# Optimization experiments

Hardware: AMD Instinct MI355X
Metric: run time of the kernel (lower is better)

## Reference

```python
import jax, jax.numpy as jnp
import numpy as np
import math

N_BITS = 8
NUM_GROUPS = 32
NUM_HEADS = 8
EPS = 1e-5


def fake_quant(x):
    # UniformAffineQuantizer: dynamic per-tensor asymmetric 8-bit fake quant
    levels = 2 ** N_BITS - 1
    xmin = jnp.minimum(x.min(), 0.0)
    xmax = jnp.maximum(x.max(), 0.0)
    scale = jnp.maximum((xmax - xmin) / levels, 1e-8)
    zp = jnp.round(-xmin / scale)
    xq = jnp.clip(jnp.round(x / scale) + zp, 0, levels)
    return (xq - zp) * scale


def group_norm(x, w, b):
    # x: (B, C, T)
    B, C, T = x.shape
    xg = x.reshape(B, NUM_GROUPS, C // NUM_GROUPS, T)
    mean = xg.mean(axis=(2, 3), keepdims=True)
    var = xg.var(axis=(2, 3), keepdims=True)
    xg = (xg - mean) * jax.lax.rsqrt(var + EPS)
    return xg.reshape(B, C, T) * w[None, :, None] + b[None, :, None]


def setup_inputs() -> dict:
    key = jax.random.key(0)
    ks = jax.random.split(key, 7)
    C = 512
    x = jax.random.normal(ks[0], (8, C, 32, 32), dtype=jnp.float32)
    gn_w = jnp.ones((C,), jnp.float32)
    gn_b = jnp.zeros((C,), jnp.float32)
    qkv_w = jax.random.normal(ks[1], (3 * C, C), jnp.float32) * (1.0 / math.sqrt(C))
    qkv_b = jax.random.normal(ks[2], (3 * C,), jnp.float32) * 0.01
    proj_w = jax.random.normal(ks[3], (C, C), jnp.float32) * (1.0 / math.sqrt(C))
    proj_b = jax.random.normal(ks[4], (C,), jnp.float32) * 0.01
    return {"x": x, "gn_w": gn_w, "gn_b": gn_b, "qkv_w": qkv_w,
            "qkv_b": qkv_b, "proj_w": proj_w, "proj_b": proj_b}


def reference(x, gn_w, gn_b, qkv_w, qkv_b, proj_w, proj_b):
    b, c, *spatial = x.shape
    T = int(np.prod(spatial))
    xf = x.reshape(b, c, T)                       # (B, C, T)
    h = group_norm(xf, gn_w, gn_b)
    qkv = jnp.einsum('oc,bct->bot', qkv_w, h) + qkv_b[None, :, None]  # (B, 3C, T)
    qkv = qkv.reshape(b * NUM_HEADS, -1, T)       # (B*H, 3*ch, T)
    ch = qkv.shape[1] // 3
    q, k, v = jnp.split(qkv, 3, axis=1)
    q = fake_quant(q)
    k = fake_quant(k)
    v = fake_quant(v)
    scale = 1.0 / math.sqrt(math.sqrt(ch))
    w = jnp.einsum('bct,bcs->bts', q * scale, k * scale)
    w = jax.nn.softmax(w.astype(jnp.float32), axis=-1).astype(q.dtype)
    a = jnp.einsum('bts,bcs->bct', w, v)          # (B*H, ch, T)
    a = a.reshape(b, c, T)
    a = jnp.einsum('oc,bct->bot', proj_w, a) + proj_b[None, :, None]
    return (xf + a).reshape(b, c, *spatial)
```

## Files before the change

### kernel.cpp

```cpp
#include <hip/hip_runtime.h>

typedef __attribute__((ext_vector_type(8))) __bf16 bf16x8;
typedef __attribute__((ext_vector_type(4))) __bf16 bf16x4;
typedef __attribute__((ext_vector_type(4))) float  f32x4;


static constexpr size_t QKV_OFF = 0;
static constexpr size_t HT_OFF  = 50331648;
static constexpr size_t WQ_OFF  = HT_OFF + 8388608;
static constexpr size_t WP_OFF  = WQ_OFF + 1572864;
static constexpr size_t MM_OFF  = WP_OFF + 524288;
static constexpr size_t GST_OFF = MM_OFF + 12288;
static constexpr size_t KI_OFF  = MM_OFF + 16384;
static constexpr size_t VI_OFF  = KI_OFF + 8388608;
static constexpr size_t NEED_NEW = VI_OFF + 8388608;

__device__ __forceinline__ float dqi(float x, float inv_s, float zp) {
    float y = rintf(x * inv_s);
    return fminf(fmaxf(y, -zp), 255.0f - zp);
}
__device__ __forceinline__ f32x4 mfma16(bf16x8 a, bf16x8 b, f32x4 c) {
    return __builtin_amdgcn_mfma_f32_16x16x32_bf16(a, b, c, 0, 0, 0);
}
__device__ __forceinline__ float exp2i(float x) {
    float r;
    asm("v_exp_f32 %0, %1" : "=v"(r) : "v"(x));
    return r;
}
__device__ __forceinline__ void glds16(const __bf16* g, __bf16* l) {
    __builtin_amdgcn_global_load_lds((const __attribute__((address_space(1))) void*)g,
                                     (__attribute__((address_space(3))) void*)l, 16, 0, 0);
}
template <int N> __device__ __forceinline__ void waitv() {
    asm volatile("s_waitcnt vmcnt(%0)" :: "n"(N) : "memory");
}
__device__ __forceinline__ void bar_raw() {
    asm volatile("s_barrier" ::: "memory");
}

__device__ __forceinline__ void red_mm(const float* __restrict__ pmm, int id, int tid,
                                       float* sred, float& mn_out, float& mx_out) {
    const float* p = pmm + id * 1024;
    float mn = fminf(p[tid * 2],     p[(tid + 256) * 2]);
    float mx = fmaxf(p[tid * 2 + 1], p[(tid + 256) * 2 + 1]);
#pragma unroll
    for (int m = 1; m < 64; m <<= 1) {
        mn = fminf(mn, __shfl_xor(mn, m));
        mx = fmaxf(mx, __shfl_xor(mx, m));
    }
    if ((tid & 63) == 0) { sred[(tid >> 6) * 2] = mn; sred[(tid >> 6) * 2 + 1] = mx; }
    __syncthreads();
    mn = fminf(fminf(sred[0], sred[2]), fminf(sred[4], sred[6]));
    mx = fmaxf(fmaxf(sred[1], sred[3]), fmaxf(sred[5], sred[7]));
    __syncthreads();
    mn_out = fminf(mn, 0.0f);
    mx_out = fmaxf(mx, 0.0f);
}

__device__ __forceinline__ void red_mm8(const float* __restrict__ pmm, int id, int tid,
                                        float* sred, float& mn_out, float& mx_out) {
    const float* p = pmm + id * 1024;
    float mn = p[tid * 2];
    float mx = p[tid * 2 + 1];
#pragma unroll
    for (int m = 1; m < 64; m <<= 1) {
        mn = fminf(mn, __shfl_xor(mn, m));
        mx = fmaxf(mx, __shfl_xor(mx, m));
    }
    if ((tid & 63) == 0) { sred[(tid >> 6) * 2] = mn; sred[(tid >> 6) * 2 + 1] = mx; }
    __syncthreads();
    float a = fminf(fminf(sred[0], sred[2]), fminf(sred[4], sred[6]));
    float b = fminf(fminf(sred[8], sred[10]), fminf(sred[12], sred[14]));
    mn = fminf(a, b);
    a = fmaxf(fmaxf(sred[1], sred[3]), fmaxf(sred[5], sred[7]));
    b = fmaxf(fmaxf(sred[9], sred[11]), fmaxf(sred[13], sred[15]));
    mx = fmaxf(a, b);
    __syncthreads();
    mn_out = fminf(mn, 0.0f);
    mx_out = fmaxf(mx, 0.0f);
}

__global__ __launch_bounds__(256) void gnstats(const float* __restrict__ x,
                                               const float* __restrict__ qw,
                                               __bf16* __restrict__ wq,
                                               const float* __restrict__ pw,
                                               __bf16* __restrict__ wp,
                                               float* __restrict__ gst) {
    int bid = blockIdx.x, tid = threadIdx.x;
    if (bid < 1024) {
        if (bid < 768) {
            int i = bid * 256 + tid;
            float4 v = ((const float4*)qw)[i];
            bf16x4 o = {(__bf16)v.x, (__bf16)v.y, (__bf16)v.z, (__bf16)v.w};
            ((bf16x4*)wq)[i] = o;
        } else {
            int i = (bid - 768) * 256 + tid;
            float4 v = ((const float4*)pw)[i];
            bf16x4 o = {(__bf16)v.x, (__bf16)v.y, (__bf16)v.z, (__bf16)v.w};
            ((bf16x4*)wp)[i] = o;
        }
        return;
    }
    int blk = bid - 1024;
    int b = blk >> 5, g = blk & 31;
    const float* xp = x + (size_t)(b * 512 + g * 16) * 1024;

    float sum = 0.f, ss = 0.f;
#pragma unroll
    for (int i = 0; i < 16; ++i) {
        float4 v = *(const float4*)(xp + (size_t)i * 1024 + tid * 4);
        sum += v.x + v.y + v.z + v.w;
        ss  += v.x * v.x + v.y * v.y + v.z * v.z + v.w * v.w;
    }
#pragma unroll
    for (int m = 1; m < 64; m <<= 1) {
        sum += __shfl_xor(sum, m);
        ss  += __shfl_xor(ss, m);
    }
    __shared__ float s1[4], s2[4];
    int wid = tid >> 6;
    if ((tid & 63) == 0) { s1[wid] = sum; s2[wid] = ss; }
    __syncthreads();
    if (tid == 0) {
        sum = s1[0] + s1[1] + s1[2] + s1[3];
        ss  = s2[0] + s2[1] + s2[2] + s2[3];
        float mean = sum * (1.0f / 16384.0f);
        float var  = ss * (1.0f / 16384.0f) - mean * mean;
        gst[blk]       = mean;
        gst[256 + blk] = rsqrtf(var + 1e-5f);
    }
}

__global__ __launch_bounds__(256) void gnapply(const float* __restrict__ x,
                                               const float* __restrict__ w,
                                               const float* __restrict__ bv,
                                               const float* __restrict__ gst,
                                               __bf16* __restrict__ hT) {
    int f = blockIdx.x;
    int b = f & 7, ts = f >> 3;
    int t0 = ts * 32;
    int tid = threadIdx.x;

    __shared__ __bf16 sH[32][520];
    int cl = tid >> 3;
    int tl = (tid & 7) * 4;

#pragma unroll
    for (int ci = 0; ci < 16; ++ci) {
        int c = ci * 32 + cl;
        int g = c >> 4;
        float mean = gst[b * 32 + g];
        float rstd = gst[256 + b * 32 + g];
        float wc = w[c] * rstd, bc = bv[c];
        float4 v = *(const float4*)(x + ((size_t)(b * 512 + c)) * 1024 + t0 + tl);
        sH[tl + 0][c] = (__bf16)((v.x - mean) * wc + bc);
        sH[tl + 1][c] = (__bf16)((v.y - mean) * wc + bc);
        sH[tl + 2][c] = (__bf16)((v.z - mean) * wc + bc);
        sH[tl + 3][c] = (__bf16)((v.w - mean) * wc + bc);
    }
    __syncthreads();
    int lane = tid & 63, wv = tid >> 6;
#pragma unroll
    for (int it = 0; it < 8; ++it) {
        int row = it * 4 + wv;
        bf16x8 o = *(const bf16x8*)&sH[row][lane * 8];
        *(bf16x8*)(hT + ((size_t)(b * 1024 + t0 + row)) * 512 + lane * 8) = o;
    }
}

template <int MTILE, int MOT, bool MINMAX, bool RESID, bool OUT16>
__global__ __launch_bounds__(256, 2) void mgemm6(const __bf16* __restrict__ A,
                                                 const __bf16* __restrict__ Bt,
                                                 const float* __restrict__ bias,
                                                 const float* __restrict__ resid,
                                                 void* __restrict__ outv,
                                                 int M, float* __restrict__ pmm) {
    constexpr int NF  = (MTILE == 128) ? 4 : 2;
    constexpr int ASZ = MTILE * 64;
    constexpr int BSZ = 128 * 64;
    constexpr int LA  = MTILE / 32;
    constexpr int L   = LA + 4;
    constexpr int STG = 2 * (ASZ + BSZ) * 2;
    constexpr int CSB = 64 * 132 * 4;
    __shared__ __attribute__((aligned(16))) char smem_raw[(STG > CSB) ? STG : CSB];
    __bf16* sA0 = (__bf16*)smem_raw;
    __bf16* sA1 = sA0 + ASZ;
    __bf16* sB0 = sA1 + ASZ;
    __bf16* sB1 = sB0 + BSZ;
    __shared__ float smn[4], smx[4];

    int tid = threadIdx.x;
    int l = tid & 63, w = tid >> 6;
    int lo = l & 15, hi = l >> 4;

    int f = blockIdx.x;
    constexpr int NWG = MOT * 64;
    int wg = (f & 7) * (NWG / 8) + (f >> 3);
    int mo = wg % MOT, nb = wg / MOT;
    int nt = nb & 7, b = nb >> 3;

    const __bf16* Ap = A + (size_t)mo * MTILE * 512;
    const __bf16* Bp = Bt + ((size_t)b * 1024 + (size_t)nt * 128) * 512;
    int m0 = (MTILE == 128) ? (w >> 1) * 64 : 0;
    int n0 = (MTILE == 128) ? (w & 1) * 64 : w * 32;
    f32x4 acc[4][NF] = {};
    int scd = tid & 7;

    auto STAGE = [&](__bf16* dA, __bf16* dB, int k0) {
#pragma unroll
        for (int p = 0; p < LA; ++p) {
            int lin = p * 2048 + tid * 8;
            int row = lin >> 6;
            glds16(Ap + (size_t)row * 512 + k0 + ((scd ^ (row & 7)) << 3), dA + lin);
        }
#pragma unroll
        for (int p = 0; p < 4; ++p) {
            int lin = p * 2048 + tid * 8;
            int row = lin >> 6;
            glds16(Bp + (size_t)row * 512 + k0 + ((scd ^ (row & 7)) << 3), dB + lin);
        }
    };
    auto COMPUTE = [&](const __bf16* cA, const __bf16* cB) {
#pragma unroll
        for (int kk = 0; kk < 2; ++kk) {
            int rch = ((kk * 4 + hi) ^ (lo & 7)) << 3;
            bf16x8 af[4], bfr[NF];
#pragma unroll
            for (int i = 0; i < 4; ++i) af[i] = *(const bf16x8*)&cA[(m0 + 16 * i + lo) * 64 + rch];
#pragma unroll
            for (int j = 0; j < NF; ++j) bfr[j] = *(const bf16x8*)&cB[(n0 + 16 * j + lo) * 64 + rch];
#pragma unroll
            for (int i = 0; i < 4; ++i)
#pragma unroll
                for (int j = 0; j < NF; ++j) acc[i][j] = mfma16(af[i], bfr[j], acc[i][j]);
        }
    };

    STAGE(sA0, sB0, 0);
#pragma unroll
    for (int kp = 0; kp < 8; kp += 2) {
        if (kp + 1 < 8) { STAGE(sA1, sB1, (kp + 1) * 64); waitv<L>(); } else { waitv<0>(); }
        bar_raw();
        COMPUTE(sA0, sB0);
        bar_raw();
        if (kp + 2 < 8) { STAGE(sA0, sB0, (kp + 2) * 64); waitv<L>(); } else { waitv<0>(); }
        bar_raw();
        COMPUTE(sA1, sB1);
        bar_raw();
    }

    float* cs = (float*)smem_raw;
    constexpr int NH = (MTILE == 128) ? 2 : 1;
#pragma unroll
    for (int h = 0; h < NH; ++h) {
        float mn = 1e30f, mx = -1e30f;
        __syncthreads();
        if (MTILE == 64 || (w >> 1) == h) {
#pragma unroll
            for (int i = 0; i < 4; ++i)
#pragma unroll
                for (int r = 0; r < 4; ++r) {
                    int rl = 16 * i + hi * 4 + r;
                    float bi = bias[mo * MTILE + h * 64 + rl];
#pragma unroll
                    for (int j = 0; j < NF; ++j)
                        cs[rl * 132 + n0 + 16 * j + lo] = acc[i][j][r] + bi;
                }
        }
        __syncthreads();
#pragma unroll
        for (int it = 0; it < 8; ++it) {
            int lin = it * 256 + tid;
            int rr = lin >> 5, cc = (lin & 31) << 2;
            float4 v = *(const float4*)&cs[rr * 132 + cc];
            if (MINMAX) {
                mn = fminf(mn, fminf(fminf(v.x, v.y), fminf(v.z, v.w)));
                mx = fmaxf(mx, fmaxf(fmaxf(v.x, v.y), fmaxf(v.z, v.w)));
            }
            int grow = mo * MTILE + h * 64 + rr;
            size_t gaddr = ((size_t)b * M + grow) * 1024 + nt * 128 + cc;
            if (RESID) {
                float4 rv = *(const float4*)&resid[gaddr];
                v.x += rv.x; v.y += rv.y; v.z += rv.z; v.w += rv.w;
            }
            if (OUT16) {
                bf16x4 o16 = {(__bf16)v.x, (__bf16)v.y, (__bf16)v.z, (__bf16)v.w};
                *(bf16x4*)&(((__bf16*)outv)[gaddr]) = o16;
            } else {
                *(float4*)&(((float*)outv)[gaddr]) = v;
            }
        }

        if (MINMAX) {
#pragma unroll
            for (int msk = 1; msk < 64; msk <<= 1) {
                mn = fminf(mn, __shfl_xor(mn, msk));
                mx = fmaxf(mx, __shfl_xor(mx, msk));
            }
            if (l == 0) { smn[w] = mn; smx[w] = mx; }
            __syncthreads();
            if (tid == 0) {
                mn = fminf(fminf(smn[0], smn[1]), fminf(smn[2], smn[3]));
                mx = fmaxf(fmaxf(smx[0], smx[1]), fmaxf(smx[2], smx[3]));
                int o = 2 * mo + h;
                int id = o % 3;
                int slot = (o / 3) * 64 + nb;
                pmm[id * 1024 + slot * 2]     = mn;
                pmm[id * 1024 + slot * 2 + 1] = mx;
            }
            __syncthreads();
        }
    }
}

__global__ __launch_bounds__(256) void quant_kv(const __bf16* __restrict__ qkv,
                                                const float* __restrict__ pmm,
                                                __bf16* __restrict__ ki,
                                                __bf16* __restrict__ vi) {
    int f = blockIdx.x;
    int b = f & 7;
    int r2 = f >> 3;
    int hh = r2 & 7, tt = r2 >> 3;
    int bh = b * 8 + hh;
    int t0 = tt * 64;
    const __bf16* kg = qkv + ((size_t)(b * 1536 + hh * 192) + 64) * 1024;
    const __bf16* vg = kg + 65536;
    int tid = threadIdx.x;

    __shared__ float sred[8];
    float mn1, mx1, mn2, mx2;
    red_mm(pmm, 1, tid, sred, mn1, mx1);
    red_mm(pmm, 2, tid, sred, mn2, mx2);
    float ksc = fmaxf((mx1 - mn1) * (1.f / 255.f), 1e-8f), kzp = rintf(-mn1 / ksc);
    float vsc = fmaxf((mx2 - mn2) * (1.f / 255.f), 1e-8f), vzp = rintf(-mn2 / vsc);
    float inv_k = 1.f / ksc, inv_v = 1.f / vsc;

    __shared__ __bf16 sT[64][68];
    int cr = tid >> 4, t4 = tid & 15;
    int s = tid >> 2, c0 = (tid & 3) * 16;

    __bf16* vd = vi + (size_t)bh * 65536;
#pragma unroll
    for (int r = 0; r < 4; ++r) {
        int c = 16 * r + cr;
        bf16x4 v = *(const bf16x4*)(vg + (size_t)c * 1024 + t0 + t4 * 4);
        bf16x4 o = {(__bf16)dqi((float)v[0], inv_v, vzp), (__bf16)dqi((float)v[1], inv_v, vzp),
                    (__bf16)dqi((float)v[2], inv_v, vzp), (__bf16)dqi((float)v[3], inv_v, vzp)};
        *(bf16x4*)(vd + (size_t)c * 1024 + t0 + t4 * 4) = o;
    }

#pragma unroll
    for (int r = 0; r < 4; ++r) {
        int c = 16 * r + cr;
        bf16x4 v = *(const bf16x4*)(kg + (size_t)c * 1024 + t0 + t4 * 4);
        sT[t4 * 4 + 0][c] = (__bf16)dqi((float)v[0], inv_k, kzp);
        sT[t4 * 4 + 1][c] = (__bf16)dqi((float)v[1], inv_k, kzp);
        sT[t4 * 4 + 2][c] = (__bf16)dqi((float)v[2], inv_k, kzp);
        sT[t4 * 4 + 3][c] = (__bf16)dqi((float)v[3], inv_k, kzp);
    }
    __syncthreads();
    bf16x8 a0 = *(const bf16x8*)&sT[s][c0];
    bf16x8 a1 = *(const bf16x8*)&sT[s][c0 + 8];
    __bf16* kd = ki + ((size_t)bh * 1024 + t0 + s) * 64 + c0;
    *(bf16x8*)kd = a0;
    *(bf16x8*)(kd + 8) = a1;
}

__global__ __launch_bounds__(512, 4) void attn5(const __bf16* __restrict__ qkv,
                                                const __bf16* __restrict__ ki,
                                                const __bf16* __restrict__ vi,
                                                const float* __restrict__ pmm,
                                                __bf16* __restrict__ aT) {
    int f = blockIdx.x;
    int bh = (f & 7) * 8 + ((f >> 3) & 7);
    int tt = f >> 6;
    int b = bh >> 3, hh = bh & 7;
    int t0 = tt * 128;
    const __bf16* qg = qkv + (size_t)(b * 1536 + hh * 192) * 1024;
    const __bf16* kb = ki + (size_t)bh * 65536;
    const __bf16* vb = vi + (size_t)bh * 65536;
    int tid = threadIdx.x;

    __shared__ float sred[16];
    float mn0, mx0, mn1, mx1, mn2, mx2;
    red_mm8(pmm, 0, tid, sred, mn0, mx0);
    red_mm8(pmm, 1, tid, sred, mn1, mx1);
    red_mm8(pmm, 2, tid, sred, mn2, mx2);
    float qsc = fmaxf((mx0 - mn0) * (1.f / 255.f), 1e-8f), qzp = rintf(-mn0 / qsc);
    float ksc = fmaxf((mx1 - mn1) * (1.f / 255.f), 1e-8f);
    float vsc = fmaxf((mx2 - mn2) * (1.f / 255.f), 1e-8f);
    float inv_q = 1.f / qsc;
    float alpha2 = qsc * ksc * 0.125f * 1.4426950408889634f;
    float thr = 11.5415603f / alpha2;

    __shared__ __bf16 sh[128][72];
    __shared__ __bf16 kS[2][4096];
    __shared__ __bf16 vS[2][4096];
    int l = tid & 63, w = tid >> 6;
    int lo = l & 15, hi = l >> 4;

    int srow = tid >> 3, sc = tid & 7;
    int swz = (sc ^ (srow & 7)) << 3;
    const __bf16* kROW = kb + (size_t)srow * 64;
    const __bf16* vROW = vb + (size_t)srow * 1024;
    int lx = lo & 7;
    int rc0 = (hi ^ lx) << 3;
    int rc1 = ((4 + hi) ^ lx) << 3;

    bf16x8 kr = *(const bf16x8*)(kROW + sc * 8);
    bf16x8 vr = *(const bf16x8*)(vROW + sc * 8);

    {
        int c0 = (tid >> 5) * 4;
        int tl = tid & 31;
#pragma unroll
        for (int r = 0; r < 4; ++r) {
            int t = tl + 32 * r;
            float y0 = dqi((float)qg[(size_t)(c0 + 0) * 1024 + t0 + t], inv_q, qzp);
            float y1 = dqi((float)qg[(size_t)(c0 + 1) * 1024 + t0 + t], inv_q, qzp);
            float y2 = dqi((float)qg[(size_t)(c0 + 2) * 1024 + t0 + t], inv_q, qzp);
            float y3 = dqi((float)qg[(size_t)(c0 + 3) * 1024 + t0 + t], inv_q, qzp);
            bf16x4 o = {(__bf16)y0, (__bf16)y1, (__bf16)y2, (__bf16)y3};
            *(bf16x4*)&sh[t][c0] = o;
        }
    }
    __syncthreads();
    bf16x8 qf0 = *(const bf16x8*)&sh[16 * w + lo][hi * 8];
    bf16x8 qf1 = *(const bf16x8*)&sh[16 * w + lo][32 + hi * 8];
    *(bf16x8*)(kS[0] + srow * 64 + swz) = kr;
    *(bf16x8*)(vS[0] + srow * 64 + swz) = vr;
    __syncthreads();

    f32x4 acc0 = {}, acc1 = {}, acc2 = {}, acc3 = {};
    float m_run = -1e30f, l_run = 0.f;

    for (int st = 0; st < 16; ++st) {
        const __bf16* kc = kS[st & 1];
        const __bf16* vc = vS[st & 1];
        if (st < 15) {
            kr = *(const bf16x8*)(kROW + (st + 1) * 4096 + sc * 8);
            vr = *(const bf16x8*)(vROW + (st + 1) * 64 + sc * 8);
        }

        f32x4 sf[4] = {};
        __builtin_amdgcn_s_setprio(1);
#pragma unroll
        for (int sm = 0; sm < 4; ++sm)
            sf[sm] = mfma16(*(const bf16x8*)(kc + (16 * sm + lo) * 64 + rc0), qf0, sf[sm]);
#pragma unroll
        for (int sm = 0; sm < 4; ++sm)
            sf[sm] = mfma16(*(const bf16x8*)(kc + (16 * sm + lo) * 64 + rc1), qf1, sf[sm]);
        __builtin_amdgcn_s_setprio(0);

        float tm = -1e30f;
#pragma unroll
        for (int sm = 0; sm < 4; ++sm) {
            float a = fmaxf(sf[sm][0], sf[sm][1]);
            float c = fmaxf(sf[sm][2], sf[sm][3]);
            tm = fmaxf(tm, fmaxf(a, c));
        }
        tm = fmaxf(tm, __shfl_xor(tm, 16));
        tm = fmaxf(tm, __shfl_xor(tm, 32));
        if (!__all(tm <= m_run + thr)) {
            float mnew = fmaxf(m_run, tm);
            float fr = exp2i(alpha2 * (m_run - mnew));
            acc0 *= fr; acc1 *= fr; acc2 *= fr; acc3 *= fr;
            l_run *= fr;
            m_run = mnew;
        }
        float cc = -alpha2 * m_run;
        float ts = 0.f;
#pragma unroll
        for (int sm = 0; sm < 4; ++sm)
#pragma unroll
            for (int r = 0; r < 4; ++r) {
                float p = exp2i(fmaf(sf[sm][r], alpha2, cc));
                sf[sm][r] = p;
                ts += p;
            }
        ts += __shfl_xor(ts, 16);
        ts += __shfl_xor(ts, 32);
        l_run += ts;

#pragma unroll
        for (int sm = 0; sm < 4; ++sm) {
            bf16x4 pb = {(__bf16)sf[sm][0], (__bf16)sf[sm][1], (__bf16)sf[sm][2], (__bf16)sf[sm][3]};
            *(bf16x4*)&sh[16 * w + lo][16 * sm + hi * 4] = pb;
        }
        bf16x8 pf0 = *(const bf16x8*)&sh[16 * w + lo][hi * 8];
        bf16x8 pf1 = *(const bf16x8*)&sh[16 * w + lo][32 + hi * 8];

        __builtin_amdgcn_s_setprio(1);
        acc0 = mfma16(*(const bf16x8*)(vc + (lo) * 64 + rc0), pf0, acc0);
        acc1 = mfma16(*(const bf16x8*)(vc + (16 + lo) * 64 + rc0), pf0, acc1);
        acc2 = mfma16(*(const bf16x8*)(vc + (32 + lo) * 64 + rc0), pf0, acc2);
        acc3 = mfma16(*(const bf16x8*)(vc + (48 + lo) * 64 + rc0), pf0, acc3);
        acc0 = mfma16(*(const bf16x8*)(vc + (lo) * 64 + rc1), pf1, acc0);
        acc1 = mfma16(*(const bf16x8*)(vc + (16 + lo) * 64 + rc1), pf1, acc1);
        acc2 = mfma16(*(const bf16x8*)(vc + (32 + lo) * 64 + rc1), pf1, acc2);
        acc3 = mfma16(*(const bf16x8*)(vc + (48 + lo) * 64 + rc1), pf1, acc3);
        __builtin_amdgcn_s_setprio(0);

        if (st < 15) {
            *(bf16x8*)(kS[(st + 1) & 1] + srow * 64 + swz) = kr;
            *(bf16x8*)(vS[(st + 1) & 1] + srow * 64 + swz) = vr;
        }
        __syncthreads();
    }

    float rl = vsc / l_run;
    {
        bf16x4 o0 = {(__bf16)(acc0[0] * rl), (__bf16)(acc0[1] * rl), (__bf16)(acc0[2] * rl), (__bf16)(acc0[3] * rl)};
        bf16x4 o1 = {(__bf16)(acc1[0] * rl), (__bf16)(acc1[1] * rl), (__bf16)(acc1[2] * rl), (__bf16)(acc1[3] * rl)};
        bf16x4 o2 = {(__bf16)(acc2[0] * rl), (__bf16)(acc2[1] * rl), (__bf16)(acc2[2] * rl), (__bf16)(acc2[3] * rl)};
        bf16x4 o3 = {(__bf16)(acc3[0] * rl), (__bf16)(acc3[1] * rl), (__bf16)(acc3[2] * rl), (__bf16)(acc3[3] * rl)};
        *(bf16x4*)&sh[16 * w + lo][0  + hi * 4] = o0;
        *(bf16x4*)&sh[16 * w + lo][16 + hi * 4] = o1;
        *(bf16x4*)&sh[16 * w + lo][32 + hi * 4] = o2;
        *(bf16x4*)&sh[16 * w + lo][48 + hi * 4] = o3;
    }
    __syncthreads();
    __bf16* ap = aT + ((size_t)b * 1024 + t0 + (tid >> 2)) * 512 + hh * 64;
    bf16x8 v0 = *(const bf16x8*)&sh[tid >> 2][(tid & 3) * 8];
    bf16x8 v1 = *(const bf16x8*)&sh[tid >> 2][32 + (tid & 3) * 8];
    *(bf16x8*)(ap + (tid & 3) * 8) = v0;
    *(bf16x8*)(ap + 32 + (tid & 3) * 8) = v1;
}

__global__ __launch_bounds__(256) void attn_mfma(const __bf16* __restrict__ qkv,
                                                 const float* __restrict__ pmm,
                                                 __bf16* __restrict__ aT) {
    int f = blockIdx.x;
    int bh = (f & 7) * 8 + ((f >> 3) & 7);
    int tt = f >> 6;
    int b = bh >> 3, hh = bh & 7;
    int t0 = tt * 64;
    const __bf16* qg = qkv + (size_t)(b * 1536 + hh * 192) * 1024;
    const __bf16* kg = qg + (size_t)64 * 1024;
    const __bf16* vg = qg + (size_t)128 * 1024;
    int tid = threadIdx.x;

    __shared__ float sred[8];
    float mn0, mx0, mn1, mx1, mn2, mx2;
    red_mm(pmm, 0, tid, sred, mn0, mx0);
    red_mm(pmm, 1, tid, sred, mn1, mx1);
    red_mm(pmm, 2, tid, sred, mn2, mx2);
    float qsc = fmaxf((mx0 - mn0) * (1.f / 255.f), 1e-8f), qzp = rintf(-mn0 / qsc);
    float ksc = fmaxf((mx1 - mn1) * (1.f / 255.f), 1e-8f), kzp = rintf(-mn1 / ksc);
    float vsc = fmaxf((mx2 - mn2) * (1.f / 255.f), 1e-8f), vzp = rintf(-mn2 / vsc);
    float inv_q = 1.f / qsc, inv_k = 1.f / ksc, inv_v = 1.f / vsc;
    float alpha = qsc * ksc * 0.125f;

    __shared__ __bf16 qT[64][72];
    __shared__ __bf16 kT[64][72];
    __shared__ __bf16 vL[64][72];
    __shared__ __bf16 pL[4][16][72];

    int l = tid & 63, w = tid >> 6;
    int lo = l & 15, hi = l >> 4;
    int c0 = (tid >> 4) * 4;
    int tl = tid & 15;

#pragma unroll
    for (int r = 0; r < 4; ++r) {
        int t = tl + 16 * r;
        float y0 = dqi((float)qg[(size_t)(c0 + 0) * 1024 + t0 + t], inv_q, qzp);
        float y1 = dqi((float)qg[(size_t)(c0 + 1) * 1024 + t0 + t], inv_q, qzp);
        float y2 = dqi((float)qg[(size_t)(c0 + 2) * 1024 + t0 + t], inv_q, qzp);
        float y3 = dqi((float)qg[(size_t)(c0 + 3) * 1024 + t0 + t], inv_q, qzp);
        bf16x4 o = {(__bf16)y0, (__bf16)y1, (__bf16)y2, (__bf16)y3};
        *(bf16x4*)&qT[t][c0] = o;
    }
    __syncthreads();
    bf16x8 qf0 = *(const bf16x8*)&qT[16 * w + lo][hi * 8];
    bf16x8 qf1 = *(const bf16x8*)&qT[16 * w + lo][32 + hi * 8];

    f32x4 acc0 = {}, acc1 = {}, acc2 = {}, acc3 = {};
    float m_run = -1e30f, l_run = 0.f;

    for (int st = 0; st < 16; ++st) {
        int s0 = st * 64;
        __syncthreads();
#pragma unroll
        for (int r = 0; r < 4; ++r) {
            int srow = tl + 16 * r;
            float y0 = dqi((float)kg[(size_t)(c0 + 0) * 1024 + s0 + srow], inv_k, kzp);
            float y1 = dqi((float)kg[(size_t)(c0 + 1) * 1024 + s0 + srow], inv_k, kzp);
            float y2 = dqi((float)kg[(size_t)(c0 + 2) * 1024 + s0 + srow], inv_k, kzp);
            float y3 = dqi((float)kg[(size_t)(c0 + 3) * 1024 + s0 + srow], inv_k, kzp);
            bf16x4 ok = {(__bf16)y0, (__bf16)y1, (__bf16)y2, (__bf16)y3};
            *(bf16x4*)&kT[srow][c0] = ok;
            int c = (tid >> 4) + 16 * r;
            bf16x4 vv = *(const bf16x4*)(vg + (size_t)c * 1024 + s0 + (tid & 15) * 4);
            bf16x4 ov = {(__bf16)dqi((float)vv[0], inv_v, vzp), (__bf16)dqi((float)vv[1], inv_v, vzp),
                         (__bf16)dqi((float)vv[2], inv_v, vzp), (__bf16)dqi((float)vv[3], inv_v, vzp)};
            *(bf16x4*)&vL[c][(tid & 15) * 4] = ov;
        }
        __syncthreads();

        f32x4 sf[4] = {};
#pragma unroll
        for (int sm = 0; sm < 4; ++sm)
            sf[sm] = mfma16(*(const bf16x8*)&kT[16 * sm + lo][hi * 8], qf0, sf[sm]);
#pragma unroll
        for (int sm = 0; sm < 4; ++sm)
            sf[sm] = mfma16(*(const bf16x8*)&kT[16 * sm + lo][32 + hi * 8], qf1, sf[sm]);

        float tm = -1e30f;
#pragma unroll
        for (int sm = 0; sm < 4; ++sm)
#pragma unroll
            for (int r = 0; r < 4; ++r) { sf[sm][r] *= alpha; tm = fmaxf(tm, sf[sm][r]); }
        tm = fmaxf(tm, __shfl_xor(tm, 16));
        tm = fmaxf(tm, __shfl_xor(tm, 32));
        float mnew = fmaxf(m_run, tm);
        float ts = 0.f;
#pragma unroll
        for (int sm = 0; sm < 4; ++sm)
#pragma unroll
            for (int r = 0; r < 4; ++r) {
                float p = __expf(sf[sm][r] - mnew);
                sf[sm][r] = p;
                ts += p;
            }
        ts += __shfl_xor(ts, 16);
        ts += __shfl_xor(ts, 32);
        float fr = __expf(m_run - mnew);
        l_run = l_run * fr + ts;
        m_run = mnew;
        acc0 *= fr; acc1 *= fr; acc2 *= fr; acc3 *= fr;

#pragma unroll
        for (int sm = 0; sm < 4; ++sm) {
            bf16x4 pb = {(__bf16)sf[sm][0], (__bf16)sf[sm][1], (__bf16)sf[sm][2], (__bf16)sf[sm][3]};
            *(bf16x4*)&pL[w][lo][16 * sm + hi * 4] = pb;
        }
        bf16x8 pf0 = *(const bf16x8*)&pL[w][lo][hi * 8];
        bf16x8 pf1 = *(const bf16x8*)&pL[w][lo][32 + hi * 8];
        acc0 = mfma16(*(const bf16x8*)&vL[lo][hi * 8], pf0, acc0);
        acc1 = mfma16(*(const bf16x8*)&vL[16 + lo][hi * 8], pf0, acc1);
        acc2 = mfma16(*(const bf16x8*)&vL[32 + lo][hi * 8], pf0, acc2);
        acc3 = mfma16(*(const bf16x8*)&vL[48 + lo][hi * 8], pf0, acc3);
        acc0 = mfma16(*(const bf16x8*)&vL[lo][32 + hi * 8], pf1, acc0);
        acc1 = mfma16(*(const bf16x8*)&vL[16 + lo][32 + hi * 8], pf1, acc1);
        acc2 = mfma16(*(const bf16x8*)&vL[32 + lo][32 + hi * 8], pf1, acc2);
        acc3 = mfma16(*(const bf16x8*)&vL[48 + lo][32 + hi * 8], pf1, acc3);
    }

    float rl = vsc / l_run;
    __syncthreads();
    {
        bf16x4 o0 = {(__bf16)(acc0[0] * rl), (__bf16)(acc0[1] * rl), (__bf16)(acc0[2] * rl), (__bf16)(acc0[3] * rl)};
        bf16x4 o1 = {(__bf16)(acc1[0] * rl), (__bf16)(acc1[1] * rl), (__bf16)(acc1[2] * rl), (__bf16)(acc1[3] * rl)};
        bf16x4 o2 = {(__bf16)(acc2[0] * rl), (__bf16)(acc2[1] * rl), (__bf16)(acc2[2] * rl), (__bf16)(acc2[3] * rl)};
        bf16x4 o3 = {(__bf16)(acc3[0] * rl), (__bf16)(acc3[1] * rl), (__bf16)(acc3[2] * rl), (__bf16)(acc3[3] * rl)};
        *(bf16x4*)&qT[16 * w + lo][0  + hi * 4] = o0;
        *(bf16x4*)&qT[16 * w + lo][16 + hi * 4] = o1;
        *(bf16x4*)&qT[16 * w + lo][32 + hi * 4] = o2;
        *(bf16x4*)&qT[16 * w + lo][48 + hi * 4] = o3;
    }
    __syncthreads();
    __bf16* ap = aT + ((size_t)b * 1024 + t0 + (tid >> 2)) * 512 + hh * 64;
    bf16x8 v0 = *(const bf16x8*)&qT[tid >> 2][(tid & 3) * 8];
    bf16x8 v1 = *(const bf16x8*)&qT[tid >> 2][32 + (tid & 3) * 8];
    *(bf16x8*)(ap + (tid & 3) * 8) = v0;
    *(bf16x8*)(ap + 32 + (tid & 3) * 8) = v1;
}

extern "C" void kernel_launch(void* const* d_in, const int* in_sizes, int n_in,
                              void* d_out, int out_size, void* d_ws, size_t ws_size,
                              hipStream_t stream) {
    const float* x      = (const float*)d_in[0];
    const float* gn_w   = (const float*)d_in[1];
    const float* gn_b   = (const float*)d_in[2];
    const float* qkv_w  = (const float*)d_in[3];
    const float* qkv_b  = (const float*)d_in[4];
    const float* proj_w = (const float*)d_in[5];
    const float* proj_b = (const float*)d_in[6];
    char* ws = (char*)d_ws;
    __bf16*   qkv16 = (__bf16*)(ws + QKV_OFF);
    __bf16*   hT  = (__bf16*)(ws + HT_OFF);
    __bf16*   wq  = (__bf16*)(ws + WQ_OFF);
    __bf16*   wp  = (__bf16*)(ws + WP_OFF);
    float*    pmm = (float*)(ws + MM_OFF);
    float*    gst = (float*)(ws + GST_OFF);
    __bf16*   ki  = (__bf16*)(ws + KI_OFF);
    __bf16*   vi  = (__bf16*)(ws + VI_OFF);
    float* out = (float*)d_out;

    gnstats<<<1280, 256, 0, stream>>>(x, qkv_w, wq, proj_w, wp, gst);
    gnapply<<<256, 256, 0, stream>>>(x, gn_w, gn_b, gst, hT);
    mgemm6<128, 12, true, false, true><<<768, 256, 0, stream>>>(wq, hT, qkv_b, nullptr, qkv16, 1536, pmm);
    if (ws_size >= NEED_NEW) {
        quant_kv<<<1024, 256, 0, stream>>>(qkv16, pmm, ki, vi);
        attn5<<<512, 512, 0, stream>>>(qkv16, ki, vi, pmm, hT);
    } else {
        attn_mfma<<<1024, 256, 0, stream>>>(qkv16, pmm, hT);
    }
    mgemm6<64, 8, false, true, false><<<512, 256, 0, stream>>>(wp, hT, proj_b, x, out, 512, nullptr);
}
```

Baseline: 86.89 us.

## Fuse V quantization into attention kernel and reorder GN stats blocks

V is no longer quantized and written to a separate buffer in the pre-pass. The attention kernel now reads raw V from the qkv buffer and quantizes each staged vector in registers before storing it to shared memory. This removes a full write and re-read of V through global memory and shrinks the pre-pass to K only, at the cost of extra ALU work inside the attention loop, repeated across the query tiles that share a head. The GN stats block order is also changed so that consecutive blocks span batches, with the output index adjusted to match.

```diff
diff --git a/kernel.cpp b/kernel.cpp
--- a/kernel.cpp
+++ b/kernel.cpp
@@ -102,7 +102,7 @@
         return;
     }
     int blk = bid - 1024;
-    int b = blk >> 5, g = blk & 31;
+    int b = blk & 7, g = blk >> 3;
     const float* xp = x + (size_t)(b * 512 + g * 16) * 1024;
 
     float sum = 0.f, ss = 0.f;
@@ -126,8 +126,9 @@
         ss  = s2[0] + s2[1] + s2[2] + s2[3];
         float mean = sum * (1.0f / 16384.0f);
         float var  = ss * (1.0f / 16384.0f) - mean * mean;
-        gst[blk]       = mean;
-        gst[256 + blk] = rsqrtf(var + 1e-5f);
+        int idx = b * 32 + g;
+        gst[idx]       = mean;
+        gst[256 + idx] = rsqrtf(var + 1e-5f);
     }
 }
 
@@ -313,10 +314,9 @@
     }
 }
 
-__global__ __launch_bounds__(256) void quant_kv(const __bf16* __restrict__ qkv,
-                                                const float* __restrict__ pmm,
-                                                __bf16* __restrict__ ki,
-                                                __bf16* __restrict__ vi) {
+__global__ __launch_bounds__(256) void quant_k(const __bf16* __restrict__ qkv,
+                                               const float* __restrict__ pmm,
+                                               __bf16* __restrict__ ki) {
     int f = blockIdx.x;
     int b = f & 7;
     int r2 = f >> 3;
@@ -324,30 +324,17 @@
     int bh = b * 8 + hh;
     int t0 = tt * 64;
     const __bf16* kg = qkv + ((size_t)(b * 1536 + hh * 192) + 64) * 1024;
-    const __bf16* vg = kg + 65536;
     int tid = threadIdx.x;
 
     __shared__ float sred[8];
-    float mn1, mx1, mn2, mx2;
+    float mn1, mx1;
     red_mm(pmm, 1, tid, sred, mn1, mx1);
-    red_mm(pmm, 2, tid, sred, mn2, mx2);
     float ksc = fmaxf((mx1 - mn1) * (1.f / 255.f), 1e-8f), kzp = rintf(-mn1 / ksc);
-    float vsc = fmaxf((mx2 - mn2) * (1.f / 255.f), 1e-8f), vzp = rintf(-mn2 / vsc);
-    float inv_k = 1.f / ksc, inv_v = 1.f / vsc;
+    float inv_k = 1.f / ksc;
 
     __shared__ __bf16 sT[64][68];
     int cr = tid >> 4, t4 = tid & 15;
     int s = tid >> 2, c0 = (tid & 3) * 16;
-
-    __bf16* vd = vi + (size_t)bh * 65536;
-#pragma unroll
-    for (int r = 0; r < 4; ++r) {
-        int c = 16 * r + cr;
-        bf16x4 v = *(const bf16x4*)(vg + (size_t)c * 1024 + t0 + t4 * 4);
-        bf16x4 o = {(__bf16)dqi((float)v[0], inv_v, vzp), (__bf16)dqi((float)v[1], inv_v, vzp),
-                    (__bf16)dqi((float)v[2], inv_v, vzp), (__bf16)dqi((float)v[3], inv_v, vzp)};
-        *(bf16x4*)(vd + (size_t)c * 1024 + t0 + t4 * 4) = o;
-    }
 
 #pragma unroll
     for (int r = 0; r < 4; ++r) {
@@ -368,7 +355,6 @@
 
 __global__ __launch_bounds__(512, 4) void attn5(const __bf16* __restrict__ qkv,
                                                 const __bf16* __restrict__ ki,
-                                                const __bf16* __restrict__ vi,
                                                 const float* __restrict__ pmm,
                                                 __bf16* __restrict__ aT) {
     int f = blockIdx.x;
@@ -378,7 +364,7 @@
     int t0 = tt * 128;
     const __bf16* qg = qkv + (size_t)(b * 1536 + hh * 192) * 1024;
     const __bf16* kb = ki + (size_t)bh * 65536;
-    const __bf16* vb = vi + (size_t)bh * 65536;
+    const __bf16* vb = qg + (size_t)128 * 1024;
     int tid = threadIdx.x;
 
     __shared__ float sred[16];
@@ -388,8 +374,8 @@
     red_mm8(pmm, 2, tid, sred, mn2, mx2);
     float qsc = fmaxf((mx0 - mn0) * (1.f / 255.f), 1e-8f), qzp = rintf(-mn0 / qsc);
     float ksc = fmaxf((mx1 - mn1) * (1.f / 255.f), 1e-8f);
-    float vsc = fmaxf((mx2 - mn2) * (1.f / 255.f), 1e-8f);
-    float inv_q = 1.f / qsc;
+    float vsc = fmaxf((mx2 - mn2) * (1.f / 255.f), 1e-8f), vzp = rintf(-mn2 / vsc);
+    float inv_q = 1.f / qsc, inv_v = 1.f / vsc;
     float alpha2 = qsc * ksc * 0.125f * 1.4426950408889634f;
     float thr = 11.5415603f / alpha2;
 
@@ -427,8 +413,13 @@
     __syncthreads();
     bf16x8 qf0 = *(const bf16x8*)&sh[16 * w + lo][hi * 8];
     bf16x8 qf1 = *(const bf16x8*)&sh[16 * w + lo][32 + hi * 8];
-    *(bf16x8*)(kS[0] + srow * 64 + swz) = kr;
-    *(bf16x8*)(vS[0] + srow * 64 + swz) = vr;
+    {
+        bf16x8 vq;
+#pragma unroll
+        for (int j = 0; j < 8; ++j) vq[j] = (__bf16)dqi((float)vr[j], inv_v, vzp);
+        *(bf16x8*)(kS[0] + srow * 64 + swz) = kr;
+        *(bf16x8*)(vS[0] + srow * 64 + swz) = vq;
+    }
     __syncthreads();
 
     f32x4 acc0 = {}, acc1 = {}, acc2 = {}, acc3 = {};
@@ -502,8 +493,11 @@
         __builtin_amdgcn_s_setprio(0);
 
         if (st < 15) {
+            bf16x8 vq;
+#pragma unroll
+            for (int j = 0; j < 8; ++j) vq[j] = (__bf16)dqi((float)vr[j], inv_v, vzp);
             *(bf16x8*)(kS[(st + 1) & 1] + srow * 64 + swz) = kr;
-            *(bf16x8*)(vS[(st + 1) & 1] + srow * 64 + swz) = vr;
+            *(bf16x8*)(vS[(st + 1) & 1] + srow * 64 + swz) = vq;
         }
         __syncthreads();
     }
@@ -685,15 +679,14 @@
     float*    pmm = (float*)(ws + MM_OFF);
     float*    gst = (float*)(ws + GST_OFF);
     __bf16*   ki  = (__bf16*)(ws + KI_OFF);
-    __bf16*   vi  = (__bf16*)(ws + VI_OFF);
     float* out = (float*)d_out;
 
     gnstats<<<1280, 256, 0, stream>>>(x, qkv_w, wq, proj_w, wp, gst);
     gnapply<<<256, 256, 0, stream>>>(x, gn_w, gn_b, gst, hT);
     mgemm6<128, 12, true, false, true><<<768, 256, 0, stream>>>(wq, hT, qkv_b, nullptr, qkv16, 1536, pmm);
     if (ws_size >= NEED_NEW) {
-        quant_kv<<<1024, 256, 0, stream>>>(qkv16, pmm, ki, vi);
-        attn5<<<512, 512, 0, stream>>>(qkv16, ki, vi, pmm, hT);
+        quant_k<<<1024, 256, 0, stream>>>(qkv16, pmm, ki);
+        attn5<<<512, 512, 0, stream>>>(qkv16, ki, pmm, hT);
     } else {
         attn_mfma<<<1024, 256, 0, stream>>>(qkv16, pmm, hT);
     }
```

After: 86.39 us. About the same (-0.6%).
